# Kernel optimization log

Measured on AMD Instinct MI355X. Metric: run time of the kernel, lower is better.

The kernel has to match this reference:

```python
import jax, jax.numpy as jnp
import numpy as np

B, S, D = 4, 2048, 128

def _phi(x, W, d):
    # original: phi(x) = (1/sqrt(M)) * exp(-0.5*||x||_2) * exp(W @ x), M = d
    proj = jnp.exp(jnp.einsum('...d,md->...m', x, W))          # [..., d]
    scale = jnp.exp(-0.5 * jnp.linalg.norm(x, axis=-1, keepdims=True))
    return (scale / jnp.sqrt(jnp.asarray(d, x.dtype))) * proj

def setup_inputs() -> dict:
    key = jax.random.key(0)
    k1, k2, k3, k4 = jax.random.split(key, 4)
    # scale 0.1 keeps exp(W @ x) well within fp32 range
    K = jax.random.normal(k1, (B, S, D), dtype=jnp.float32) * 0.1
    Q = jax.random.normal(k2, (B, S, D), dtype=jnp.float32) * 0.1
    V = jax.random.normal(k3, (B, S, D), dtype=jnp.float32) * 0.1
    W_phi = jax.random.normal(k4, (D, D), dtype=jnp.float32)
    sent_embed_slice = jnp.zeros((B, 1), dtype=jnp.float32)
    return {"K": K, "Q": Q, "V": V, "sent_embed_slice": sent_embed_slice,
            "max_seq_length": S, "qkv_size": D, "W_phi": W_phi}

def reference(K, Q, V, sent_embed_slice, max_seq_length, qkv_size, W_phi):
    d = qkv_size
    phiK = _phi(K, W_phi, d)   # [B, S, d]
    phiQ = _phi(Q, W_phi, d)   # [B, S, d]
    Bn = K.shape[0]

    def step(carry, inp):
        Mst, Nst = carry                       # [B, d, d], [B, d]
        pk, v, pq = inp                        # each [B, d]
        Mst = Mst + pk[:, :, None] * v[:, None, :]   # cumulative outer product
        Nst = Nst + pk                               # cumulative feature sum
        num = jnp.einsum('bd,bde->be', pq, Mst)      # phi(q) @ M
        r = jnp.einsum('bd,bd->b', pq, Nst)          # phi(q) . N
        out = num / (r + jnp.sign(r) * 1e-6)[:, None]
        return (Mst, Nst), out

    init = (jnp.zeros((Bn, d, d), K.dtype), jnp.zeros((Bn, d), K.dtype))
    xs = (jnp.swapaxes(phiK, 0, 1), jnp.swapaxes(V, 0, 1), jnp.swapaxes(phiQ, 0, 1))
    _, outs = jax.lax.scan(step, init, xs)    # outs: [S, B, d]
    return jnp.swapaxes(outs, 0, 1)           # [B, S, d]
```

## Files before the change

### kernel.cpp

```cpp
#include <hip/hip_runtime.h>

typedef float v4 __attribute__((ext_vector_type(4)));
typedef float v2 __attribute__((ext_vector_type(2)));
typedef short s8v __attribute__((ext_vector_type(8)));
typedef float f4v __attribute__((ext_vector_type(4)));
typedef unsigned short u16;
typedef u16 us2 __attribute__((ext_vector_type(2)));
typedef u16 us4 __attribute__((ext_vector_type(4)));
typedef u16 us8 __attribute__((ext_vector_type(8)));

#define OFF_PHIKB 0
#define OFF_PHIQB 524288
#define OFF_KVTB  1048576
#define OFF_PMB   2097152
#define OFF_N32   3145728
#define OFF_PN    3162112

__device__ inline u16 f2bf(float f) {
  union { float f; unsigned u; } v; v.f = f;
  unsigned r = v.u + 0x7fffu + ((v.u >> 16) & 1u);
  return (u16)(r >> 16);
}
__device__ inline float bf2f(u16 h) {
  union { unsigned u; float f; } v; v.u = ((unsigned)h) << 16; return v.f;
}

__global__ __launch_bounds__(512) void phikv_kernel(
    const float* __restrict__ K, const float* __restrict__ Q,
    const float* __restrict__ V, const float* __restrict__ W,
    u16* __restrict__ phiKb, u16* __restrict__ phiQb,
    u16* __restrict__ KVTb, float* __restrict__ N32) {
  __shared__ __align__(16) u16 smem[27136];
  __shared__ float srowsq[64];
  __shared__ float scl[64];
  u16* Xb = smem;
  u16* Wb = smem + 8704;
  u16* Pb = smem;
  u16* KdT = smem + 8704;
  u16* Vt = smem + 17920;

  const int tid = threadIdx.x;
  const bool isK = (blockIdx.y == 0);
  const float* X = isK ? K : Q;
  u16* outPhi = isK ? phiKb : phiQb;
  const int row0 = blockIdx.x * 64;
  const int wv = tid >> 6;
  const int lane = tid & 63;
  const int q = lane >> 4;
  const int ln = lane & 15;

  v4 vpa[2], vpb[2];
  if (isK) {
#pragma unroll
    for (int k = 0; k < 2; k++) {
      int j = tid + k * 512;
      int s0 = (j & 31) * 2;
      int e4 = (j >> 5) * 4;
      vpa[k] = *(const v4*)&V[(size_t)(row0 + s0) * 128 + e4];
      vpb[k] = *(const v4*)&V[(size_t)(row0 + s0 + 1) * 128 + e4];
    }
  }

#pragma unroll
  for (int k = 0; k < 4; k++) {
    int j = tid + k * 512;
    int r = j >> 5;
    int c4 = (j & 31) * 4;
    v4 x = *(const v4*)&X[(size_t)(row0 + r) * 128 + c4];
    us4 xb;
    float p = 0.f;
#pragma unroll
    for (int i = 0; i < 4; i++) { xb[i] = f2bf(x[i]); p += x[i] * x[i]; }
    *(us4*)&Xb[r * 136 + c4] = xb;
    p += __shfl_down(p, 16, 32);
    p += __shfl_down(p, 8, 32);
    p += __shfl_down(p, 4, 32);
    p += __shfl_down(p, 2, 32);
    p += __shfl_down(p, 1, 32);
    if ((tid & 31) == 0) srowsq[r] = p;
  }
#pragma unroll
  for (int k = 0; k < 8; k++) {
    int j = tid + k * 512;
    int r = j >> 5;
    int c4 = (j & 31) * 4;
    v4 w = *(const v4*)&W[(size_t)r * 128 + c4];
    us4 wb;
#pragma unroll
    for (int i = 0; i < 4; i++) wb[i] = f2bf(w[i]);
    *(us4*)&Wb[r * 136 + c4] = wb;
  }
  __syncthreads();
  if (tid < 64)
    scl[tid] = 0.08838834764831845f * __expf(-0.5f * sqrtf(srowsq[tid]));

  const int tr = wv >> 1;
  const int cb = (wv & 1) * 4;
  f4v acc[4];
#pragma unroll
  for (int i = 0; i < 4; i++) acc[i] = (f4v){0.f, 0.f, 0.f, 0.f};
#pragma unroll
  for (int ks = 0; ks < 4; ks++) {
    s8v a = *(const s8v*)&Xb[(tr * 16 + ln) * 136 + ks * 32 + q * 8];
#pragma unroll
    for (int i = 0; i < 4; i++) {
      s8v bb = *(const s8v*)&Wb[((cb + i) * 16 + ln) * 136 + ks * 32 + q * 8];
      acc[i] = __builtin_amdgcn_mfma_f32_16x16x32_bf16(a, bb, acc[i], 0, 0, 0);
    }
  }
  __syncthreads();

#pragma unroll
  for (int i = 0; i < 4; i++) {
    const int ct = cb + i;
    us4 col;
#pragma unroll
    for (int r = 0; r < 4; r++) {
      int row = tr * 16 + q * 4 + r;
      u16 hv = f2bf(scl[row] * __expf(acc[i][r]));
      Pb[row * 136 + ct * 16 + ln] = hv;
      col[r] = hv;
    }
    if (isK) *(us4*)&KdT[(ct * 16 + ln) * 72 + tr * 16 + q * 4] = col;
  }
  if (isK) {
#pragma unroll
    for (int k = 0; k < 2; k++) {
      int j = tid + k * 512;
      int s0 = (j & 31) * 2;
      int e4 = (j >> 5) * 4;
#pragma unroll
      for (int i = 0; i < 4; i++) {
        us2 w2 = {f2bf(vpa[k][i]), f2bf(vpb[k][i])};
        *(us2*)&Vt[(e4 + i) * 72 + s0] = w2;
      }
    }
  }
  __syncthreads();

#pragma unroll
  for (int k = 0; k < 2; k++) {
    int j = tid + k * 512;
    int r = j >> 4;
    int d8 = (j & 15) * 8;
    *(us8*)&outPhi[(size_t)(row0 + r) * 128 + d8] = *(const us8*)&Pb[r * 136 + d8];
  }
  if (!isK) return;

  const int b = row0 >> 11;
  const int c = (row0 >> 6) & 31;

  if (tid < 128) {
    float ns = 0.f;
#pragma unroll
    for (int s = 0; s < 64; s++) ns += bf2f(KdT[tid * 72 + s]);
    N32[(size_t)(b * 32 + c) * 128 + tid] = ns;
  }

  {
    const int et = wv;
    s8v a0 = *(const s8v*)&Vt[(et * 16 + ln) * 72 + q * 8];
    s8v a1 = *(const s8v*)&Vt[(et * 16 + ln) * 72 + 32 + q * 8];
    f4v ac[8];
#pragma unroll
    for (int dt = 0; dt < 8; dt++) ac[dt] = (f4v){0.f, 0.f, 0.f, 0.f};
#pragma unroll
    for (int dt = 0; dt < 8; dt++) {
      s8v b0 = *(const s8v*)&KdT[(dt * 16 + ln) * 72 + q * 8];
      ac[dt] = __builtin_amdgcn_mfma_f32_16x16x32_bf16(a0, b0, ac[dt], 0, 0, 0);
      s8v b1 = *(const s8v*)&KdT[(dt * 16 + ln) * 72 + 32 + q * 8];
      ac[dt] = __builtin_amdgcn_mfma_f32_16x16x32_bf16(a1, b1, ac[dt], 0, 0, 0);
    }
#pragma unroll
    for (int dt = 0; dt < 8; dt++)
#pragma unroll
      for (int r = 0; r < 4; r++) {
        int e = et * 16 + q * 4 + r;
        int d = dt * 16 + ln;
        KVTb[((size_t)(b * 128 + e) * 32 + c) * 128 + d] = f2bf(ac[dt][r]);
      }
  }
}

__global__ __launch_bounds__(256) void prefix_kernel(
    const u16* __restrict__ KVTb, const float* __restrict__ N32,
    u16* __restrict__ PMb, float* __restrict__ PN) {
  const int tid = threadIdx.x;
  const int bid = blockIdx.x;
  if (bid < 64) {
    const int r = bid * 8 + (tid >> 5);
    const int d4 = (tid & 31) * 4;
    const size_t base = (size_t)r * (32 * 128);
    float acc[4] = {0.f, 0.f, 0.f, 0.f};
#pragma unroll 4
    for (int c = 0; c < 32; c++) {
      us4 st;
#pragma unroll
      for (int i = 0; i < 4; i++) st[i] = f2bf(acc[i]);
      *(us4*)&PMb[base + c * 128 + d4] = st;
      us4 kv = *(const us4*)&KVTb[base + c * 128 + d4];
#pragma unroll
      for (int i = 0; i < 4; i++) acc[i] += bf2f(kv[i]);
    }
  } else {
    const int b = tid >> 6;
    const int d2 = (tid & 63) * 2;
    float a0 = 0.f, a1 = 0.f;
#pragma unroll 4
    for (int c = 0; c < 32; c++) {
      size_t idx = (size_t)(b * 32 + c) * 128 + d2;
      *(v2*)&PN[idx] = (v2){a0, a1};
      v2 nv = *(const v2*)&N32[idx];
      a0 += nv[0];
      a1 += nv[1];
    }
  }
}

__global__ __launch_bounds__(256) void out_kernel(
    const u16* __restrict__ phiKb, const u16* __restrict__ phiQb,
    const float* __restrict__ V, const u16* __restrict__ PMb,
    const float* __restrict__ PN, float* __restrict__ out) {
  __shared__ __align__(16) u16 Qs[64 * 136];
  __shared__ __align__(16) u16 Ks[64 * 136];
  __shared__ __align__(16) u16 Ms[32 * 136];
  __shared__ __align__(16) u16 Vt[32 * 72];
  __shared__ __align__(16) u16 Ps[64 * 72];
  __shared__ float Ns[128];
  __shared__ float rs[64];

  const int tid = threadIdx.x;
  const int id = blockIdx.x;
  const int h = id & 3;
  const int c = (id >> 2) & 31;
  const int b = id >> 7;
  const int srow0 = b * 2048 + c * 64;
  const int ecol0 = h * 32;
  const int wv = tid >> 6;
  const int lane = tid & 63;
  const int q = lane >> 4;
  const int ln = lane & 15;

  const int vs0 = (tid & 31) * 2;
  const int ve4 = (tid >> 5) * 4;
  v4 va = *(const v4*)&V[(size_t)(srow0 + vs0) * 128 + ecol0 + ve4];
  v4 vb = *(const v4*)&V[(size_t)(srow0 + vs0 + 1) * 128 + ecol0 + ve4];

#pragma unroll
  for (int k = 0; k < 4; k++) {
    int j = tid + k * 256;
    int t = j >> 4;
    int d8 = (j & 15) * 8;
    *(us8*)&Qs[t * 136 + d8] = *(const us8*)&phiQb[(size_t)(srow0 + t) * 128 + d8];
    *(us8*)&Ks[t * 136 + d8] = *(const us8*)&phiKb[(size_t)(srow0 + t) * 128 + d8];
  }
#pragma unroll
  for (int k = 0; k < 2; k++) {
    int j = tid + k * 256;
    int e = j >> 4;
    int d8 = (j & 15) * 8;
    *(us8*)&Ms[e * 136 + d8] =
        *(const us8*)&PMb[((size_t)(b * 128 + ecol0 + e) * 32 + c) * 128 + d8];
  }
  if (tid < 128) Ns[tid] = PN[(size_t)(b * 32 + c) * 128 + tid];
#pragma unroll
  for (int i = 0; i < 4; i++) {
    us2 w2 = {f2bf(va[i]), f2bf(vb[i])};
    *(us2*)&Vt[(ve4 + i) * 72 + vs0] = w2;
  }
  __syncthreads();

  {
    const int tr = wv;
    for (int tc = 0; tc < 4; tc++) {
      f4v acc = {0.f, 0.f, 0.f, 0.f};
      if (tc <= tr) {
#pragma unroll
        for (int ks = 0; ks < 4; ks++) {
          s8v a = *(const s8v*)&Qs[(tr * 16 + ln) * 136 + ks * 32 + q * 8];
          s8v bb = *(const s8v*)&Ks[(tc * 16 + ln) * 136 + ks * 32 + q * 8];
          acc = __builtin_amdgcn_mfma_f32_16x16x32_bf16(a, bb, acc, 0, 0, 0);
        }
      }
      const int s_g = tc * 16 + ln;
#pragma unroll
      for (int r = 0; r < 4; r++) {
        int t_g = tr * 16 + q * 4 + r;
        Ps[t_g * 72 + s_g] = f2bf(s_g <= t_g ? acc[r] : 0.f);
      }
    }
  }
  __syncthreads();

  {
    const int t = tid >> 2;
    const int p4 = tid & 3;
    float rsl = 0.f;
#pragma unroll
    for (int s = p4; s < 64; s += 4) rsl += bf2f(Ps[t * 72 + s]);
#pragma unroll
    for (int d = p4; d < 128; d += 4) rsl += bf2f(Qs[t * 136 + d]) * Ns[d];
    rsl += __shfl_down(rsl, 2, 4);
    rsl += __shfl_down(rsl, 1, 4);
    if (p4 == 0) rs[t] = rsl;
  }

  const int et = wv & 1;
  f4v acc2[2];
#pragma unroll
  for (int i = 0; i < 2; i++) acc2[i] = (f4v){0.f, 0.f, 0.f, 0.f};
#pragma unroll
  for (int i = 0; i < 2; i++) {
    const int tr2 = (wv >> 1) + 2 * i;
#pragma unroll
    for (int ks2 = 0; ks2 < 2; ks2++) {
      s8v a_p = *(const s8v*)&Ps[(tr2 * 16 + ln) * 72 + ks2 * 32 + q * 8];
      s8v b_v = *(const s8v*)&Vt[(et * 16 + ln) * 72 + ks2 * 32 + q * 8];
      acc2[i] = __builtin_amdgcn_mfma_f32_16x16x32_bf16(a_p, b_v, acc2[i], 0, 0, 0);
    }
#pragma unroll
    for (int ks = 0; ks < 4; ks++) {
      s8v a_q = *(const s8v*)&Qs[(tr2 * 16 + ln) * 136 + ks * 32 + q * 8];
      s8v b_m = *(const s8v*)&Ms[(et * 16 + ln) * 136 + ks * 32 + q * 8];
      acc2[i] = __builtin_amdgcn_mfma_f32_16x16x32_bf16(a_q, b_m, acc2[i], 0, 0, 0);
    }
  }
  __syncthreads();

#pragma unroll
  for (int i = 0; i < 2; i++) {
    const int tr2 = (wv >> 1) + 2 * i;
#pragma unroll
    for (int r = 0; r < 4; r++) {
      int t_g = tr2 * 16 + q * 4 + r;
      float rv = rs[t_g];
      float den = rv + (rv > 0.f ? 1e-6f : (rv < 0.f ? -1e-6f : 0.f));
      out[(size_t)(srow0 + t_g) * 128 + ecol0 + et * 16 + ln] =
          acc2[i][r] / den;
    }
  }
}

extern "C" void kernel_launch(void* const* d_in, const int* in_sizes, int n_in,
                              void* d_out, int out_size, void* d_ws,
                              size_t ws_size, hipStream_t stream) {
  (void)in_sizes; (void)n_in; (void)out_size; (void)ws_size;
  const float* K = (const float*)d_in[0];
  const float* Q = (const float*)d_in[1];
  const float* V = (const float*)d_in[2];
  const float* W = (const float*)d_in[6];
  float* out = (float*)d_out;
  float* ws = (float*)d_ws;

  u16* phiKb = (u16*)(ws + OFF_PHIKB);
  u16* phiQb = (u16*)(ws + OFF_PHIQB);
  u16* KVTb = (u16*)(ws + OFF_KVTB);
  u16* PMb = (u16*)(ws + OFF_PMB);
  float* N32 = ws + OFF_N32;
  float* PN = ws + OFF_PN;

  phikv_kernel<<<dim3(128, 2), 512, 0, stream>>>(K, Q, V, W, phiKb, phiQb,
                                                 KVTb, N32);
  prefix_kernel<<<65, 256, 0, stream>>>(KVTb, N32, PMb, PN);
  out_kernel<<<512, 256, 0, stream>>>(phiKb, phiQb, V, PMb, PN, out);
}
```

Baseline: 94.00 us.

## Fuse chunk prefix-sum into output kernel and drop separate prefix launch

Removes the separate prefix_kernel. Each output block now sums the per-chunk KV and N partials of all earlier chunks itself, reading KVTb and N32 directly. Block-to-chunk order is reversed so the blocks with the most prefix work are scheduled first. This saves one launch and the PMb/PN round trip through global memory. In exchange it adds redundant loads and summation across blocks, up to 31 chunks per block, with uneven load between blocks.

```diff
diff --git a/kernel.cpp b/kernel.cpp
--- a/kernel.cpp
+++ b/kernel.cpp
@@ -1,7 +1,6 @@
 #include <hip/hip_runtime.h>
 
 typedef float v4 __attribute__((ext_vector_type(4)));
-typedef float v2 __attribute__((ext_vector_type(2)));
 typedef short s8v __attribute__((ext_vector_type(8)));
 typedef float f4v __attribute__((ext_vector_type(4)));
 typedef unsigned short u16;
@@ -12,9 +11,7 @@
 #define OFF_PHIKB 0
 #define OFF_PHIQB 524288
 #define OFF_KVTB  1048576
-#define OFF_PMB   2097152
-#define OFF_N32   3145728
-#define OFF_PN    3162112
+#define OFF_N32   2097152
 
 __device__ inline u16 f2bf(float f) {
   union { float f; unsigned u; } v; v.f = f;
@@ -182,45 +179,10 @@
   }
 }
 
-__global__ __launch_bounds__(256) void prefix_kernel(
-    const u16* __restrict__ KVTb, const float* __restrict__ N32,
-    u16* __restrict__ PMb, float* __restrict__ PN) {
-  const int tid = threadIdx.x;
-  const int bid = blockIdx.x;
-  if (bid < 64) {
-    const int r = bid * 8 + (tid >> 5);
-    const int d4 = (tid & 31) * 4;
-    const size_t base = (size_t)r * (32 * 128);
-    float acc[4] = {0.f, 0.f, 0.f, 0.f};
-#pragma unroll 4
-    for (int c = 0; c < 32; c++) {
-      us4 st;
-#pragma unroll
-      for (int i = 0; i < 4; i++) st[i] = f2bf(acc[i]);
-      *(us4*)&PMb[base + c * 128 + d4] = st;
-      us4 kv = *(const us4*)&KVTb[base + c * 128 + d4];
-#pragma unroll
-      for (int i = 0; i < 4; i++) acc[i] += bf2f(kv[i]);
-    }
-  } else {
-    const int b = tid >> 6;
-    const int d2 = (tid & 63) * 2;
-    float a0 = 0.f, a1 = 0.f;
-#pragma unroll 4
-    for (int c = 0; c < 32; c++) {
-      size_t idx = (size_t)(b * 32 + c) * 128 + d2;
-      *(v2*)&PN[idx] = (v2){a0, a1};
-      v2 nv = *(const v2*)&N32[idx];
-      a0 += nv[0];
-      a1 += nv[1];
-    }
-  }
-}
-
 __global__ __launch_bounds__(256) void out_kernel(
     const u16* __restrict__ phiKb, const u16* __restrict__ phiQb,
-    const float* __restrict__ V, const u16* __restrict__ PMb,
-    const float* __restrict__ PN, float* __restrict__ out) {
+    const float* __restrict__ V, const u16* __restrict__ KVTb,
+    const float* __restrict__ N32, float* __restrict__ out) {
   __shared__ __align__(16) u16 Qs[64 * 136];
   __shared__ __align__(16) u16 Ks[64 * 136];
   __shared__ __align__(16) u16 Ms[32 * 136];
@@ -232,7 +194,7 @@
   const int tid = threadIdx.x;
   const int id = blockIdx.x;
   const int h = id & 3;
-  const int c = (id >> 2) & 31;
+  const int c = 31 - ((id >> 2) & 31);
   const int b = id >> 7;
   const int srow0 = b * 2048 + c * 64;
   const int ecol0 = h * 32;
@@ -254,15 +216,38 @@
     *(us8*)&Qs[t * 136 + d8] = *(const us8*)&phiQb[(size_t)(srow0 + t) * 128 + d8];
     *(us8*)&Ks[t * 136 + d8] = *(const us8*)&phiKb[(size_t)(srow0 + t) * 128 + d8];
   }
-#pragma unroll
-  for (int k = 0; k < 2; k++) {
-    int j = tid + k * 256;
-    int e = j >> 4;
-    int d8 = (j & 15) * 8;
-    *(us8*)&Ms[e * 136 + d8] =
-        *(const us8*)&PMb[((size_t)(b * 128 + ecol0 + e) * 32 + c) * 128 + d8];
-  }
-  if (tid < 128) Ns[tid] = PN[(size_t)(b * 32 + c) * 128 + tid];
+
+  {
+    const int se = tid >> 4;
+    const int sd8 = (tid & 15) * 8;
+    const u16* src0 =
+        &KVTb[((size_t)(b * 128 + ecol0 + se) * 32) * 128 + sd8];
+    const u16* src1 =
+        &KVTb[((size_t)(b * 128 + ecol0 + 16 + se) * 32) * 128 + sd8];
+    float m0[8], m1[8];
+#pragma unroll
+    for (int i = 0; i < 8; i++) { m0[i] = 0.f; m1[i] = 0.f; }
+    for (int cp = 0; cp < c; cp++) {
+      us8 k0 = *(const us8*)&src0[cp * 128];
+      us8 k1 = *(const us8*)&src1[cp * 128];
+#pragma unroll
+      for (int i = 0; i < 8; i++) {
+        m0[i] += bf2f(k0[i]);
+        m1[i] += bf2f(k1[i]);
+      }
+    }
+    us8 w0, w1;
+#pragma unroll
+    for (int i = 0; i < 8; i++) { w0[i] = f2bf(m0[i]); w1[i] = f2bf(m1[i]); }
+    *(us8*)&Ms[se * 136 + sd8] = w0;
+    *(us8*)&Ms[(16 + se) * 136 + sd8] = w1;
+  }
+  if (tid < 128) {
+    float na = 0.f;
+    for (int cp = 0; cp < c; cp++)
+      na += N32[(size_t)(b * 32 + cp) * 128 + tid];
+    Ns[tid] = na;
+  }
 #pragma unroll
   for (int i = 0; i < 4; i++) {
     us2 w2 = {f2bf(va[i]), f2bf(vb[i])};
@@ -355,12 +340,9 @@
   u16* phiKb = (u16*)(ws + OFF_PHIKB);
   u16* phiQb = (u16*)(ws + OFF_PHIQB);
   u16* KVTb = (u16*)(ws + OFF_KVTB);
-  u16* PMb = (u16*)(ws + OFF_PMB);
   float* N32 = ws + OFF_N32;
-  float* PN = ws + OFF_PN;
 
   phikv_kernel<<<dim3(128, 2), 512, 0, stream>>>(K, Q, V, W, phiKb, phiQb,
                                                  KVTb, N32);
-  prefix_kernel<<<65, 256, 0, stream>>>(KVTb, N32, PMb, PN);
-  out_kernel<<<512, 256, 0, stream>>>(phiKb, phiQb, V, PMb, PN, out);
-}
+  out_kernel<<<512, 256, 0, stream>>>(phiKb, phiQb, V, KVTb, N32, out);
+}
```

Result: slower. 103.8 us (+10.4%).
